# Optimization experiments

Hardware: AMD Instinct MI355X
Metric: run time of the kernel (lower is better)

The kernel has to match this reference:

```python
import jax, jax.numpy as jnp
import numpy as np

D_MODEL = 1024
NUM_HEADS = 16
D_K = D_MODEL // NUM_HEADS
SCALE = float(np.sqrt(D_K))


def setup_inputs() -> dict:
    key = jax.random.key(0)
    ks = jax.random.split(key, 12)
    B, S = 4, 2048
    s = 1.0 / np.sqrt(D_MODEL)
    inp = {
        'query': jax.random.normal(ks[0], (B, S, D_MODEL), jnp.float32),
        'key':   jax.random.normal(ks[1], (B, S, D_MODEL), jnp.float32),
        'value': jax.random.normal(ks[2], (B, S, D_MODEL), jnp.float32),
        'Wq': jax.random.normal(ks[3], (D_MODEL, D_MODEL), jnp.float32) * s,
        'bq': jax.random.normal(ks[4], (D_MODEL,), jnp.float32) * s,
        'Wk': jax.random.normal(ks[5], (D_MODEL, D_MODEL), jnp.float32) * s,
        'bk': jax.random.normal(ks[6], (D_MODEL,), jnp.float32) * s,
        'Wv': jax.random.normal(ks[7], (D_MODEL, D_MODEL), jnp.float32) * s,
        'bv': jax.random.normal(ks[8], (D_MODEL,), jnp.float32) * s,
        'Wo': jax.random.normal(ks[9], (D_MODEL, D_MODEL), jnp.float32) * s,
        'bo': jax.random.normal(ks[10], (D_MODEL,), jnp.float32) * s,
    }
    return inp


def reference(query, key, value, Wq, bq, Wk, bk, Wv, bv, Wo, bo):
    B, Sq, _ = query.shape
    Skv = key.shape[1]
    # torch Linear: x @ W.T + b
    def proj(x, W, b, S):
        y = jnp.einsum('bsd,ed->bse', x, W) + b
        return y.reshape(B, S, NUM_HEADS, D_K).transpose(0, 2, 1, 3)  # [B,H,S,dk]
    Q = proj(query, Wq, bq, Sq)
    K = proj(key, Wk, bk, Skv)
    V = proj(value, Wv, bv, Skv)
    scores = jnp.einsum('bhqd,bhkd->bhqk', Q, K) / SCALE  # [B,H,Sq,Skv]
    attn = jax.nn.softmax(scores, axis=-1)  # dropout=0 -> identity
    out = jnp.einsum('bhqk,bhkd->bhqd', attn, V)
    out = out.transpose(0, 2, 1, 3).reshape(B, Sq, D_MODEL)
    out = jnp.einsum('bsd,ed->bse', out, Wo) + bo
    return out
```

## Files before the change

### kernel.cpp

```cpp
#include <hip/hip_runtime.h>


typedef __attribute__((ext_vector_type(8))) __bf16 bf16x8;
typedef __attribute__((ext_vector_type(4))) __bf16 bf16x4;
typedef __attribute__((ext_vector_type(4))) float f32x4;

#define SCALE_FOLD 0.18033688011112043f

__device__ __forceinline__ void async_copy16(const void* g, void* lds) {
  __builtin_amdgcn_global_load_lds(
      (const __attribute__((address_space(1))) void*)g,
      (__attribute__((address_space(3))) void*)lds, 16, 0, 0);
}

template <int ROWS>
__device__ __forceinline__ void stage_tile(const __bf16* __restrict__ g, int ld,
                                           __bf16* lds, int tid) {
  const int wave_base = tid & ~63;
#pragma unroll
  for (int r = 0; r < ROWS / 32; ++r) {
    int slot = r * 256 + tid;
    int row = slot >> 3;
    int c = slot & 7;
    int gc = c ^ (row & 7);
    async_copy16(g + row * ld + gc * 8, lds + (r * 256 + wave_base) * 8);
  }
}

__device__ __forceinline__ bf16x8 frag_ld(const __bf16* lds, int row, int chunk) {
  return *(const bf16x8*)(lds + row * 64 + ((chunk ^ (row & 7)) << 3));
}

__global__ void cvt_all(const float* __restrict__ s0, const float* __restrict__ s1,
                        const float* __restrict__ s2, const float* __restrict__ s3,
                        const float* __restrict__ s4, const float* __restrict__ s5,
                        const float* __restrict__ s6, __bf16* d0, __bf16* d1,
                        __bf16* d2, __bf16* d3, __bf16* d4, __bf16* d5,
                        __bf16* d6, int n4_big, int n4_small) {
  const int z = blockIdx.y;
  const float* src;
  __bf16* dst;
  int n4;
  switch (z) {
    case 0: src = s0; dst = d0; n4 = n4_big; break;
    case 1: src = s1; dst = d1; n4 = n4_big; break;
    case 2: src = s2; dst = d2; n4 = n4_big; break;
    case 3: src = s3; dst = d3; n4 = n4_small; break;
    case 4: src = s4; dst = d4; n4 = n4_small; break;
    case 5: src = s5; dst = d5; n4 = n4_small; break;
    default: src = s6; dst = d6; n4 = n4_small; break;
  }
  int i = blockIdx.x * blockDim.x + threadIdx.x;
  if (i < n4) {
    float4 v = ((const float4*)src)[i];
    bf16x4 o = {(__bf16)v.x, (__bf16)v.y, (__bf16)v.z, (__bf16)v.w};
    ((bf16x4*)dst)[i] = o;
  }
}

__device__ __forceinline__ void gemm_body(const __bf16* __restrict__ A,
                                          const __bf16* __restrict__ B,
                                          const float* __restrict__ bias,
                                          void* __restrict__ out, int K,
                                          int mode, int m0, int n0,
                                          __bf16* Alds, __bf16* Blds) {
  const int tid = threadIdx.x;
  const int lane = tid & 63;
  const int w = tid >> 6;
  const int wm = w >> 1, wn = w & 1;
  const int l15 = lane & 15, quad = lane >> 4;

  f32x4 acc[4][4] = {};

  for (int k0 = 0; k0 < K; k0 += 64) {
    stage_tile<128>(A + m0 * K + k0, K, Alds, tid);
    stage_tile<128>(B + n0 * K + k0, K, Blds, tid);
    __syncthreads();
#pragma unroll
    for (int kc = 0; kc < 2; ++kc) {
      bf16x8 af[4], bfr[4];
#pragma unroll
      for (int mi = 0; mi < 4; ++mi)
        af[mi] = frag_ld(Alds, wm * 64 + mi * 16 + l15, kc * 4 + quad);
#pragma unroll
      for (int ni = 0; ni < 4; ++ni)
        bfr[ni] = frag_ld(Blds, wn * 64 + ni * 16 + l15, kc * 4 + quad);
#pragma unroll
      for (int mi = 0; mi < 4; ++mi)
#pragma unroll
        for (int ni = 0; ni < 4; ++ni)
          acc[mi][ni] = __builtin_amdgcn_mfma_f32_16x16x32_bf16(
              af[mi], bfr[ni], acc[mi][ni], 0, 0, 0);
    }
    __syncthreads();
  }

#pragma unroll
  for (int mi = 0; mi < 4; ++mi) {
#pragma unroll
    for (int i = 0; i < 4; ++i) {
      int grow = m0 + wm * 64 + mi * 16 + quad * 4 + i;
#pragma unroll
      for (int ni = 0; ni < 4; ++ni) {
        int gcol = n0 + wn * 64 + ni * 16 + l15;
        float v = acc[mi][ni][i];
        if (mode == 3) {
          v += bias[gcol];
          ((float*)out)[grow * 1024 + gcol] = v;
        } else if (mode == 2) {
          v += bias[grow];
          int h = grow >> 6, dd = grow & 63;
          int b = gcol >> 11, s = gcol & 2047;
          ((__bf16*)out)[(((b * 16 + h) * 64 + dd) * 2048) + s] = (__bf16)v;
        } else {
          v += bias[gcol];
          if (mode == 0) v *= SCALE_FOLD;
          int h = gcol >> 6, dd = gcol & 63;
          int b = grow >> 11, s = grow & 2047;
          ((__bf16*)out)[(((b * 16 + h) * 2048 + s) * 64) + dd] = (__bf16)v;
        }
      }
    }
  }
}

__device__ __forceinline__ void remap_xcd(int lid, int& mblk, int& nblk) {
  int xcd = lid & 7;
  int j = lid >> 3;
  mblk = xcd * 8 + (j >> 3);
  nblk = j & 7;
}

__global__ __launch_bounds__(256) void gemm_qkv(
    const __bf16* __restrict__ xq, const __bf16* __restrict__ xk,
    const __bf16* __restrict__ xv, const __bf16* __restrict__ wq,
    const __bf16* __restrict__ wk, const __bf16* __restrict__ wv,
    const float* __restrict__ bq, const float* __restrict__ bk,
    const float* __restrict__ bv, __bf16* Qb, __bf16* Kb, __bf16* Vtb) {
  __shared__ alignas(16) __bf16 Alds[128 * 64];
  __shared__ alignas(16) __bf16 Blds[128 * 64];
  int mblk, nblk;
  remap_xcd(blockIdx.x, mblk, nblk);
  const int z = blockIdx.y;
  if (z == 0) {
    gemm_body(xq, wq, bq, Qb, 1024, 0, mblk * 128, nblk * 128, Alds, Blds);
  } else if (z == 1) {
    gemm_body(xk, wk, bk, Kb, 1024, 1, mblk * 128, nblk * 128, Alds, Blds);
  } else {
    gemm_body(wv, xv, bv, Vtb, 1024, 2, nblk * 128, mblk * 128, Alds, Blds);
  }
}

__global__ __launch_bounds__(256) void gemm_out(const __bf16* __restrict__ A,
                                                const __bf16* __restrict__ B,
                                                const float* __restrict__ bias,
                                                float* __restrict__ out) {
  __shared__ alignas(16) __bf16 Alds[128 * 64];
  __shared__ alignas(16) __bf16 Blds[128 * 64];
  int mblk, nblk;
  remap_xcd(blockIdx.x, mblk, nblk);
  gemm_body(A, B, bias, out, 1024, 3, mblk * 128, nblk * 128, Alds, Blds);
}

__global__ __launch_bounds__(256) void attn_kernel(
    const __bf16* __restrict__ Qg, const __bf16* __restrict__ Kg,
    const __bf16* __restrict__ Vt, __bf16* __restrict__ AO) {
  __shared__ alignas(16) __bf16 Klds[2][64 * 64];
  __shared__ alignas(16) __bf16 Vlds[2][64 * 64];
  __shared__ alignas(16) __bf16 Plds[4][32 * 64];

  const int tid = threadIdx.x;
  const int lane = tid & 63;
  const int w = tid >> 6;
  const int l15 = lane & 15, quad = lane >> 4;
  const int S = 2048;

  const int bid = blockIdx.x;
  const int r = bid >> 3;
  const int bh = (bid & 7) * 8 + (r & 7);
  const int q0 = (r >> 3) * 128;

  const __bf16* Qbase = Qg + (size_t)bh * S * 64;
  const __bf16* Kbase = Kg + (size_t)bh * S * 64;
  const __bf16* Vbase = Vt + (size_t)bh * 64 * S;

  stage_tile<128>(Qbase + q0 * 64, 64, (__bf16*)Klds, tid);
  __syncthreads();
  bf16x8 qf[2][2];
#pragma unroll
  for (int qi = 0; qi < 2; ++qi)
#pragma unroll
    for (int kc = 0; kc < 2; ++kc)
      qf[qi][kc] =
          frag_ld((__bf16*)Klds, w * 32 + qi * 16 + l15, kc * 4 + quad);
  __syncthreads();

  stage_tile<64>(Kbase, 64, Klds[0], tid);
  stage_tile<64>(Vbase, S, Vlds[0], tid);
  __syncthreads();

  const bf16x8 ones = {__bf16(1.f), __bf16(1.f), __bf16(1.f), __bf16(1.f),
                       __bf16(1.f), __bf16(1.f), __bf16(1.f), __bf16(1.f)};

  f32x4 oacc[2][4] = {};
  f32x4 lacc[2] = {};
  __bf16* Pw = Plds[w];

  for (int mt = 0; mt < 32; ++mt) {
    const int cur = mt & 1;
    if (mt + 1 < 32) {
      stage_tile<64>(Kbase + (mt + 1) * 64 * 64, 64, Klds[cur ^ 1], tid);
      stage_tile<64>(Vbase + (mt + 1) * 64, S, Vlds[cur ^ 1], tid);
    }

    f32x4 sacc[4][2] = {};
#pragma unroll
    for (int kc = 0; kc < 2; ++kc) {
      bf16x8 kf[4];
#pragma unroll
      for (int ci = 0; ci < 4; ++ci)
        kf[ci] = frag_ld(Klds[cur], ci * 16 + l15, kc * 4 + quad);
#pragma unroll
      for (int ci = 0; ci < 4; ++ci)
#pragma unroll
        for (int qi = 0; qi < 2; ++qi)
          sacc[ci][qi] = __builtin_amdgcn_mfma_f32_16x16x32_bf16(
              kf[ci], qf[qi][kc], sacc[ci][qi], 0, 0, 0);
    }

#pragma unroll
    for (int ci = 0; ci < 4; ++ci) {
#pragma unroll
      for (int qi = 0; qi < 2; ++qi) {
        bf16x4 pk;
#pragma unroll
        for (int i = 0; i < 4; ++i)
          pk[i] = (__bf16)__builtin_amdgcn_exp2f(sacc[ci][qi][i]);
        int qrow = qi * 16 + l15;
        int chunk = 2 * ci + (quad >> 1);
        int addr = qrow * 64 + ((chunk ^ (qrow & 7)) << 3) + ((quad & 1) << 2);
        *(bf16x4*)(Pw + addr) = pk;
      }
    }

#pragma unroll
    for (int kc = 0; kc < 2; ++kc) {
      bf16x8 pf[2], vf[4];
#pragma unroll
      for (int mi = 0; mi < 2; ++mi)
        pf[mi] = frag_ld(Pw, mi * 16 + l15, kc * 4 + quad);
#pragma unroll
      for (int ni = 0; ni < 4; ++ni)
        vf[ni] = frag_ld(Vlds[cur], ni * 16 + l15, kc * 4 + quad);
#pragma unroll
      for (int mi = 0; mi < 2; ++mi)
        lacc[mi] = __builtin_amdgcn_mfma_f32_16x16x32_bf16(pf[mi], ones,
                                                           lacc[mi], 0, 0, 0);
#pragma unroll
      for (int mi = 0; mi < 2; ++mi)
#pragma unroll
        for (int ni = 0; ni < 4; ++ni)
          oacc[mi][ni] = __builtin_amdgcn_mfma_f32_16x16x32_bf16(
              pf[mi], vf[ni], oacc[mi][ni], 0, 0, 0);
    }
    __syncthreads();
  }

  const int b = bh >> 4;
  const int hh = bh & 15;
#pragma unroll
  for (int mi = 0; mi < 2; ++mi) {
#pragma unroll
    for (int i = 0; i < 4; ++i) {
      int s = q0 + w * 32 + mi * 16 + quad * 4 + i;
      float inv_l = 1.f / lacc[mi][i];
#pragma unroll
      for (int ni = 0; ni < 4; ++ni) {
        int d = ni * 16 + l15;
        AO[((size_t)(b * 2048 + s)) * 1024 + hh * 64 + d] =
            (__bf16)(oacc[mi][ni][i] * inv_l);
      }
    }
  }
}

extern "C" void kernel_launch(void* const* d_in, const int* in_sizes, int n_in,
                              void* d_out, int out_size, void* d_ws,
                              size_t ws_size, hipStream_t stream) {
  const float* q_in = (const float*)d_in[0];
  const float* k_in = (const float*)d_in[1];
  const float* v_in = (const float*)d_in[2];
  const float* Wq = (const float*)d_in[3];
  const float* bq = (const float*)d_in[4];
  const float* Wk = (const float*)d_in[5];
  const float* bk = (const float*)d_in[6];
  const float* Wv = (const float*)d_in[7];
  const float* bv = (const float*)d_in[8];
  const float* Wo = (const float*)d_in[9];
  const float* bo = (const float*)d_in[10];

  const size_t SZ_X = (size_t)8192 * 1024 * 2;
  const size_t SZ_W = (size_t)1024 * 1024 * 2;
  char* p = (char*)d_ws;
  __bf16* xq = (__bf16*)p; p += SZ_X;
  __bf16* xk = (__bf16*)p; p += SZ_X;
  __bf16* xv = (__bf16*)p; p += SZ_X;
  __bf16* wqb = (__bf16*)p; p += SZ_W;
  __bf16* wkb = (__bf16*)p; p += SZ_W;
  __bf16* wvb = (__bf16*)p; p += SZ_W;
  __bf16* wob = (__bf16*)p; p += SZ_W;
  __bf16* Qb = (__bf16*)p; p += SZ_X;
  __bf16* Kb = (__bf16*)p; p += SZ_X;
  __bf16* Vtb = (__bf16*)p; p += SZ_X;
  __bf16* AOb = (__bf16*)p; p += SZ_X;

  const int nx4 = 8192 * 1024 / 4, nw4 = 1024 * 1024 / 4;
  cvt_all<<<dim3(nx4 / 256, 7), 256, 0, stream>>>(
      q_in, k_in, v_in, Wq, Wk, Wv, Wo, xq, xk, xv, wqb, wkb, wvb, wob, nx4,
      nw4);

  gemm_qkv<<<dim3(512, 3), 256, 0, stream>>>(xq, xk, xv, wqb, wkb, wvb, bq,
                                             bk, bv, Qb, Kb, Vtb);

  attn_kernel<<<1024, 256, 0, stream>>>(Qb, Kb, Vtb, AOb);

  gemm_out<<<512, 256, 0, stream>>>(AOb, wob, bo, (float*)d_out);
}
```

Baseline: 342.5 us.

## Keep P in registers via 16x16x16 MFMA and use two-wave attention blocks

The attention kernel now feeds the exp'd score accumulators straight into 16x16x16 bf16 MFMAs as the A operand for the PV product and row-sum. This removes the per-wave P staging buffer in LDS and its write/read round trip. Blocks shrink to 128 threads, with each wave covering 64 query rows, so every staged K/V tile is reused by more rows per wave. The cost is more registers per wave, more V fragment reads using narrow 8-byte LDS loads, and fewer waves per block to hide latency.

```diff
diff --git a/kernel.cpp b/kernel.cpp
--- a/kernel.cpp
+++ b/kernel.cpp
@@ -4,6 +4,7 @@
 typedef __attribute__((ext_vector_type(8))) __bf16 bf16x8;
 typedef __attribute__((ext_vector_type(4))) __bf16 bf16x4;
 typedef __attribute__((ext_vector_type(4))) float f32x4;
+typedef __attribute__((ext_vector_type(4))) short s16x4;
 
 #define SCALE_FOLD 0.18033688011112043f
 
@@ -13,17 +14,17 @@
       (__attribute__((address_space(3))) void*)lds, 16, 0, 0);
 }
 
-template <int ROWS>
+template <int ROWS, int THREADS>
 __device__ __forceinline__ void stage_tile(const __bf16* __restrict__ g, int ld,
                                            __bf16* lds, int tid) {
   const int wave_base = tid & ~63;
 #pragma unroll
-  for (int r = 0; r < ROWS / 32; ++r) {
-    int slot = r * 256 + tid;
+  for (int r = 0; r < ROWS * 8 / THREADS; ++r) {
+    int slot = r * THREADS + tid;
     int row = slot >> 3;
     int c = slot & 7;
     int gc = c ^ (row & 7);
-    async_copy16(g + row * ld + gc * 8, lds + (r * 256 + wave_base) * 8);
+    async_copy16(g + row * ld + gc * 8, lds + (r * THREADS + wave_base) * 8);
   }
 }
 
@@ -73,8 +74,8 @@
   f32x4 acc[4][4] = {};
 
   for (int k0 = 0; k0 < K; k0 += 64) {
-    stage_tile<128>(A + m0 * K + k0, K, Alds, tid);
-    stage_tile<128>(B + n0 * K + k0, K, Blds, tid);
+    stage_tile<128, 256>(A + m0 * K + k0, K, Alds, tid);
+    stage_tile<128, 256>(B + n0 * K + k0, K, Blds, tid);
     __syncthreads();
 #pragma unroll
     for (int kc = 0; kc < 2; ++kc) {
@@ -162,12 +163,11 @@
   gemm_body(A, B, bias, out, 1024, 3, mblk * 128, nblk * 128, Alds, Blds);
 }
 
-__global__ __launch_bounds__(256) void attn_kernel(
+__global__ __launch_bounds__(128, 2) void attn_kernel(
     const __bf16* __restrict__ Qg, const __bf16* __restrict__ Kg,
     const __bf16* __restrict__ Vt, __bf16* __restrict__ AO) {
   __shared__ alignas(16) __bf16 Klds[2][64 * 64];
   __shared__ alignas(16) __bf16 Vlds[2][64 * 64];
-  __shared__ alignas(16) __bf16 Plds[4][32 * 64];
 
   const int tid = threadIdx.x;
   const int lane = tid & 63;
@@ -184,36 +184,34 @@
   const __bf16* Kbase = Kg + (size_t)bh * S * 64;
   const __bf16* Vbase = Vt + (size_t)bh * 64 * S;
 
-  stage_tile<128>(Qbase + q0 * 64, 64, (__bf16*)Klds, tid);
+  stage_tile<128, 128>(Qbase + q0 * 64, 64, (__bf16*)Klds, tid);
   __syncthreads();
-  bf16x8 qf[2][2];
-#pragma unroll
-  for (int qi = 0; qi < 2; ++qi)
+  bf16x8 qf[4][2];
+#pragma unroll
+  for (int qi = 0; qi < 4; ++qi)
 #pragma unroll
     for (int kc = 0; kc < 2; ++kc)
       qf[qi][kc] =
-          frag_ld((__bf16*)Klds, w * 32 + qi * 16 + l15, kc * 4 + quad);
+          frag_ld((__bf16*)Klds, w * 64 + qi * 16 + l15, kc * 4 + quad);
   __syncthreads();
 
-  stage_tile<64>(Kbase, 64, Klds[0], tid);
-  stage_tile<64>(Vbase, S, Vlds[0], tid);
+  stage_tile<64, 128>(Kbase, 64, Klds[0], tid);
+  stage_tile<64, 128>(Vbase, S, Vlds[0], tid);
   __syncthreads();
 
-  const bf16x8 ones = {__bf16(1.f), __bf16(1.f), __bf16(1.f), __bf16(1.f),
-                       __bf16(1.f), __bf16(1.f), __bf16(1.f), __bf16(1.f)};
-
-  f32x4 oacc[2][4] = {};
-  f32x4 lacc[2] = {};
-  __bf16* Pw = Plds[w];
+  const s16x4 ones = {0x3F80, 0x3F80, 0x3F80, 0x3F80};
+
+  f32x4 oacc[4][4] = {};
+  f32x4 lacc[4] = {};
 
   for (int mt = 0; mt < 32; ++mt) {
     const int cur = mt & 1;
     if (mt + 1 < 32) {
-      stage_tile<64>(Kbase + (mt + 1) * 64 * 64, 64, Klds[cur ^ 1], tid);
-      stage_tile<64>(Vbase + (mt + 1) * 64, S, Vlds[cur ^ 1], tid);
-    }
-
-    f32x4 sacc[4][2] = {};
+      stage_tile<64, 128>(Kbase + (mt + 1) * 64 * 64, 64, Klds[cur ^ 1], tid);
+      stage_tile<64, 128>(Vbase + (mt + 1) * 64, S, Vlds[cur ^ 1], tid);
+    }
+
+    f32x4 sacc[4][4] = {};
 #pragma unroll
     for (int kc = 0; kc < 2; ++kc) {
       bf16x8 kf[4];
@@ -223,45 +221,35 @@
 #pragma unroll
       for (int ci = 0; ci < 4; ++ci)
 #pragma unroll
-        for (int qi = 0; qi < 2; ++qi)
+        for (int qi = 0; qi < 4; ++qi)
           sacc[ci][qi] = __builtin_amdgcn_mfma_f32_16x16x32_bf16(
               kf[ci], qf[qi][kc], sacc[ci][qi], 0, 0, 0);
     }
 
 #pragma unroll
     for (int ci = 0; ci < 4; ++ci) {
-#pragma unroll
-      for (int qi = 0; qi < 2; ++qi) {
+      s16x4 vfs[4];
+#pragma unroll
+      for (int ni = 0; ni < 4; ++ni) {
+        int row = ni * 16 + l15;
+        int c0 = ci * 16 + quad * 4;
+        int addr = row * 64 + (((c0 >> 3) ^ (row & 7)) << 3) + (c0 & 7);
+        vfs[ni] = *(const s16x4*)(Vlds[cur] + addr);
+      }
+#pragma unroll
+      for (int qi = 0; qi < 4; ++qi) {
         bf16x4 pk;
 #pragma unroll
         for (int i = 0; i < 4; ++i)
           pk[i] = (__bf16)__builtin_amdgcn_exp2f(sacc[ci][qi][i]);
-        int qrow = qi * 16 + l15;
-        int chunk = 2 * ci + (quad >> 1);
-        int addr = qrow * 64 + ((chunk ^ (qrow & 7)) << 3) + ((quad & 1) << 2);
-        *(bf16x4*)(Pw + addr) = pk;
+        s16x4 pks = __builtin_bit_cast(s16x4, pk);
+        lacc[qi] = __builtin_amdgcn_mfma_f32_16x16x16bf16_1k(pks, ones,
+                                                             lacc[qi], 0, 0, 0);
+#pragma unroll
+        for (int ni = 0; ni < 4; ++ni)
+          oacc[qi][ni] = __builtin_amdgcn_mfma_f32_16x16x16bf16_1k(
+              pks, vfs[ni], oacc[qi][ni], 0, 0, 0);
       }
-    }
-
-#pragma unroll
-    for (int kc = 0; kc < 2; ++kc) {
-      bf16x8 pf[2], vf[4];
-#pragma unroll
-      for (int mi = 0; mi < 2; ++mi)
-        pf[mi] = frag_ld(Pw, mi * 16 + l15, kc * 4 + quad);
-#pragma unroll
-      for (int ni = 0; ni < 4; ++ni)
-        vf[ni] = frag_ld(Vlds[cur], ni * 16 + l15, kc * 4 + quad);
-#pragma unroll
-      for (int mi = 0; mi < 2; ++mi)
-        lacc[mi] = __builtin_amdgcn_mfma_f32_16x16x32_bf16(pf[mi], ones,
-                                                           lacc[mi], 0, 0, 0);
-#pragma unroll
-      for (int mi = 0; mi < 2; ++mi)
-#pragma unroll
-        for (int ni = 0; ni < 4; ++ni)
-          oacc[mi][ni] = __builtin_amdgcn_mfma_f32_16x16x32_bf16(
-              pf[mi], vf[ni], oacc[mi][ni], 0, 0, 0);
     }
     __syncthreads();
   }
@@ -269,16 +257,16 @@
   const int b = bh >> 4;
   const int hh = bh & 15;
 #pragma unroll
-  for (int mi = 0; mi < 2; ++mi) {
+  for (int qi = 0; qi < 4; ++qi) {
 #pragma unroll
     for (int i = 0; i < 4; ++i) {
-      int s = q0 + w * 32 + mi * 16 + quad * 4 + i;
-      float inv_l = 1.f / lacc[mi][i];
+      int s = q0 + w * 64 + qi * 16 + quad * 4 + i;
+      float inv_l = 1.f / lacc[qi][i];
 #pragma unroll
       for (int ni = 0; ni < 4; ++ni) {
         int d = ni * 16 + l15;
         AO[((size_t)(b * 2048 + s)) * 1024 + hh * 64 + d] =
-            (__bf16)(oacc[mi][ni][i] * inv_l);
+            (__bf16)(oacc[qi][ni][i] * inv_l);
       }
     }
   }
@@ -322,7 +310,7 @@
   gemm_qkv<<<dim3(512, 3), 256, 0, stream>>>(xq, xk, xv, wqb, wkb, wvb, bq,
                                              bk, bv, Qb, Kb, Vtb);
 
-  attn_kernel<<<1024, 256, 0, stream>>>(Qb, Kb, Vtb, AOb);
+  attn_kernel<<<1024, 128, 0, stream>>>(Qb, Kb, Vtb, AOb);
 
   gemm_out<<<512, 256, 0, stream>>>(AOb, wob, bo, (float*)d_out);
 }
```

Result: faster. 330.2 us (-3.6%).
